# Kernel optimization log

Hardware: AMD Instinct MI355X
Metric: run time of the kernel (lower is better)

## Reference

```python
import jax, jax.numpy as jnp
import numpy as np

N_NODES = 100000
N_EDGES = 1600000
D = 128


def setup_inputs() -> dict:
    key = jax.random.key(0)
    ks = jax.random.split(key, 12)
    x = jax.random.normal(ks[0], (N_NODES, D), dtype=jnp.float32)
    edge_index = jax.random.randint(ks[1], (2, N_EDGES), 0, N_NODES, dtype=jnp.int64)
    s = 1.0 / np.sqrt(D)
    params = {}
    for i in range(3):
        params[f"Wl{i}"] = jax.random.uniform(ks[2 + 3 * i], (D, D), jnp.float32, -s, s)
        params[f"bl{i}"] = jax.random.uniform(ks[3 + 3 * i], (D,), jnp.float32, -s, s)
        params[f"Wr{i}"] = jax.random.uniform(ks[4 + 3 * i], (D, D), jnp.float32, -s, s)
    return {"x": x, "edge_index": edge_index, **params}


def _sage_conv(x, src, dst, Wl, bl, Wr):
    # mean-aggregate neighbor features: out_i = mean_{j: (j->i)} x_j
    msg = x[src]                                              # [E, D] gather
    agg = jax.ops.segment_sum(msg, dst, num_segments=N_NODES)  # [N, D]
    deg = jax.ops.segment_sum(jnp.ones_like(dst, dtype=x.dtype), dst, num_segments=N_NODES)
    agg = agg / jnp.maximum(deg, 1.0)[:, None]
    # PyG SAGEConv: lin_l(aggregated) + lin_r(x); lin_r has no bias
    return agg @ Wl + bl + x @ Wr


def reference(x, edge_index, Wl0, bl0, Wr0, Wl1, bl1, Wr1, Wl2, bl2, Wr2):
    src, dst = edge_index[0], edge_index[1]
    # layer 0 + relu (dropout is identity in eval mode)
    h = jax.nn.relu(_sage_conv(x, src, dst, Wl0, bl0, Wr0))
    # layer 1 + relu
    h = jax.nn.relu(_sage_conv(h, src, dst, Wl1, bl1, Wr1))
    # final layer, no activation
    return _sage_conv(h, src, dst, Wl2, bl2, Wr2)
```

## Files before the change

kernel.cpp:

```cpp
#include <hip/hip_runtime.h>
#include <hip/hip_bf16.h>

#define NN 100000
#define NE 1600000
#define DD 128

typedef __attribute__((ext_vector_type(8))) short bf16x8;
typedef __attribute__((ext_vector_type(4))) float f32x4;

__device__ __forceinline__ float bfu2f(unsigned short u) {
    unsigned v = ((unsigned)u) << 16;
    return __builtin_bit_cast(float, v);
}
__device__ __forceinline__ unsigned short f2bf(float f) {
    unsigned u = __builtin_bit_cast(unsigned, f);
    u += 0x7fffu + ((u >> 16) & 1u);
    return (unsigned short)(u >> 16);
}
__device__ __forceinline__ void split2(float v, unsigned short& hi, unsigned short& lo) {
    hi = f2bf(v);
    lo = f2bf(v - bfu2f(hi));
}
__device__ __forceinline__ float lo_f(unsigned u) { return __builtin_bit_cast(float, u << 16); }
__device__ __forceinline__ float hi_f(unsigned u) { return __builtin_bit_cast(float, u & 0xffff0000u); }

__global__ __launch_bounds__(256) void detect_kernel(const int* __restrict__ ei,
                                                     int* __restrict__ flag) {
    __shared__ int red[256];
    int t = threadIdx.x;
    int v = 0;
    for (int i = t; i < 4096; i += 256) v |= ei[2 * i + 1];
    red[t] = v;
    __syncthreads();
    for (int s = 128; s > 0; s >>= 1) {
        if (t < s) red[t] |= red[t + s];
        __syncthreads();
    }
    if (t == 0) flag[0] = (red[0] == 0) ? 1 : 0;
}

__device__ __forceinline__ int eidx(const int* __restrict__ ei, int idx, int is64) {
    return is64 ? ei[2 * idx] : ei[idx];
}

__global__ __launch_bounds__(256) void count_deg(const int* __restrict__ ei,
                                                 const int* __restrict__ flag,
                                                 int* __restrict__ deg) {
    int e = blockIdx.x * 256 + threadIdx.x;
    if (e < NE) {
        int is64 = flag[0];
        int dst = eidx(ei, NE + e, is64);
        atomicAdd(&deg[dst], 1);
    }
}

__global__ __launch_bounds__(1024) void scan_excl(const int* __restrict__ deg,
                                                  int* __restrict__ ptr) {
    __shared__ int wsum[16];
    __shared__ int carry_s;
    int t = threadIdx.x;
    int lane = t & 63, w = t >> 6;
    if (t == 0) carry_s = 0;
    __syncthreads();
    for (int base = 0; base < NN; base += 1024) {
        int i = base + t;
        int v = (i < NN) ? deg[i] : 0;
        int x = v;
        #pragma unroll
        for (int off = 1; off < 64; off <<= 1) {
            int y = __shfl_up(x, off, 64);
            if (lane >= off) x += y;
        }
        if (lane == 63) wsum[w] = x;
        __syncthreads();
        if (w == 0) {
            int s = (lane < 16) ? wsum[lane] : 0;
            #pragma unroll
            for (int off = 1; off < 16; off <<= 1) {
                int y = __shfl_up(s, off, 64);
                if (lane >= off) s += y;
            }
            if (lane < 16) wsum[lane] = s;
        }
        __syncthreads();
        int carry = carry_s;
        int woff = (w == 0) ? 0 : wsum[w - 1];
        if (i < NN) ptr[i] = carry + woff + (x - v);
        int chunk_total = wsum[15];
        __syncthreads();
        if (t == 0) carry_s = carry + chunk_total;
        __syncthreads();
    }
    if (threadIdx.x == 0) ptr[NN] = carry_s;
}

__global__ __launch_bounds__(256) void init_aux(const int* __restrict__ deg,
                                                const int* __restrict__ ptr,
                                                float* __restrict__ invd,
                                                int* __restrict__ cursor) {
    int i = blockIdx.x * 256 + threadIdx.x;
    if (i < NN) {
        int d = deg[i];
        invd[i] = 1.0f / (float)(d > 1 ? d : 1);
        cursor[i] = ptr[i];
    }
}

__global__ __launch_bounds__(256) void fill_csr(const int* __restrict__ ei,
                                                const int* __restrict__ flag,
                                                int* __restrict__ cursor,
                                                int* __restrict__ csre) {
    int e = blockIdx.x * 256 + threadIdx.x;
    if (e < NE) {
        int is64 = flag[0];
        int dst = eidx(ei, NE + e, is64);
        int src = eidx(ei, e, is64);
        int pos = atomicAdd(&cursor[dst], 1);
        csre[pos] = src;
    }
}

__global__ __launch_bounds__(256) void convert_x(const float* __restrict__ x,
                                                 unsigned* __restrict__ xh,
                                                 unsigned* __restrict__ xl) {
    int i = blockIdx.x * 256 + threadIdx.x;
    if (i >= NN * 64) return;
    float2 v = ((const float2*)x)[i];
    unsigned short h0, l0, h1, l1;
    split2(v.x, h0, l0);
    split2(v.y, h1, l1);
    xh[i] = (unsigned)h0 | ((unsigned)h1 << 16);
    xl[i] = (unsigned)l0 | ((unsigned)l1 << 16);
}

__global__ __launch_bounds__(256) void convert_w(const float* __restrict__ Wlm,
                                                 const float* __restrict__ Wrm,
                                                 unsigned short* __restrict__ Wth,
                                                 unsigned short* __restrict__ Wtl) {
    int i = blockIdx.x * 256 + threadIdx.x;
    if (i >= 128 * 256) return;
    int n = i >> 8, k = i & 255;
    float v = (k < 128) ? Wlm[k * 128 + n] : Wrm[(k - 128) * 128 + n];
    unsigned short h, l;
    split2(v, h, l);
    Wth[i] = h;
    Wtl[i] = l;
}

__global__ __launch_bounds__(256) void aggregate_bf(const unsigned* __restrict__ Hh,
                                                    const unsigned* __restrict__ Hl,
                                                    const int* __restrict__ csre,
                                                    const int* __restrict__ ptr,
                                                    const float* __restrict__ invd,
                                                    unsigned* __restrict__ Ah,
                                                    unsigned* __restrict__ Al) {
    int gw = blockIdx.x * 4 + (threadIdx.x >> 6);
    int lane = threadIdx.x & 63;
    if (gw >= NN) return;
    int beg = ptr[gw], end = ptr[gw + 1];
    float s00 = 0.f, s01 = 0.f, s10 = 0.f, s11 = 0.f;
    float s20 = 0.f, s21 = 0.f, s30 = 0.f, s31 = 0.f;
    int j = beg;
    for (; j + 4 <= end; j += 4) {
        int i0 = csre[j], i1 = csre[j + 1], i2 = csre[j + 2], i3 = csre[j + 3];
        unsigned h0 = Hh[(size_t)i0 * 64 + lane], g0 = Hl[(size_t)i0 * 64 + lane];
        unsigned h1 = Hh[(size_t)i1 * 64 + lane], g1 = Hl[(size_t)i1 * 64 + lane];
        unsigned h2 = Hh[(size_t)i2 * 64 + lane], g2 = Hl[(size_t)i2 * 64 + lane];
        unsigned h3 = Hh[(size_t)i3 * 64 + lane], g3 = Hl[(size_t)i3 * 64 + lane];
        s00 += lo_f(h0) + lo_f(g0); s01 += hi_f(h0) + hi_f(g0);
        s10 += lo_f(h1) + lo_f(g1); s11 += hi_f(h1) + hi_f(g1);
        s20 += lo_f(h2) + lo_f(g2); s21 += hi_f(h2) + hi_f(g2);
        s30 += lo_f(h3) + lo_f(g3); s31 += hi_f(h3) + hi_f(g3);
    }
    for (; j < end; ++j) {
        int i0 = csre[j];
        unsigned h0 = Hh[(size_t)i0 * 64 + lane], g0 = Hl[(size_t)i0 * 64 + lane];
        s00 += lo_f(h0) + lo_f(g0);
        s01 += hi_f(h0) + hi_f(g0);
    }
    float s = invd[gw];
    float v0 = ((s00 + s10) + (s20 + s30)) * s;
    float v1 = ((s01 + s11) + (s21 + s31)) * s;
    unsigned short h0_, l0_, h1_, l1_;
    split2(v0, h0_, l0_);
    split2(v1, h1_, l1_);
    Ah[(size_t)gw * 64 + lane] = (unsigned)h0_ | ((unsigned)h1_ << 16);
    Al[(size_t)gw * 64 + lane] = (unsigned)l0_ | ((unsigned)l1_ << 16);
}

__global__ __launch_bounds__(256) void gemm_mfma(const unsigned short* __restrict__ A0h,
                                                 const unsigned short* __restrict__ A0l,
                                                 const unsigned short* __restrict__ A1h,
                                                 const unsigned short* __restrict__ A1l,
                                                 const unsigned short* __restrict__ Wh,
                                                 const unsigned short* __restrict__ Wl_,
                                                 const float* __restrict__ bias,
                                                 unsigned short* __restrict__ Oh,
                                                 unsigned short* __restrict__ Ol,
                                                 float* __restrict__ Of,
                                                 int mode) {
    int t = threadIdx.x;
    int w = t >> 6, l = t & 63;
    int lr = l & 15, lh = l >> 4;
    int m0 = blockIdx.x * 64 + w * 16;
    int ra = m0 + lr;
    if (ra >= NN) ra = NN - 1;
    const char* pa0h = (const char*)A0h + (size_t)ra * 256;
    const char* pa0l = (const char*)A0l + (size_t)ra * 256;
    const char* pa1h = (const char*)A1h + (size_t)ra * 256;
    const char* pa1l = (const char*)A1l + (size_t)ra * 256;
    bf16x8 ah[8], al[8];
    #pragma unroll
    for (int s = 0; s < 4; ++s) {
        int off = s * 64 + lh * 16;
        ah[s]     = *(const bf16x8*)(pa0h + off);
        al[s]     = *(const bf16x8*)(pa0l + off);
        ah[s + 4] = *(const bf16x8*)(pa1h + off);
        al[s + 4] = *(const bf16x8*)(pa1l + off);
    }
    #pragma unroll
    for (int ct = 0; ct < 8; ++ct) {
        int colr = ct * 16 + lr;
        const char* pbh = (const char*)Wh + (size_t)colr * 512;
        const char* pbl = (const char*)Wl_ + (size_t)colr * 512;
        f32x4 acc = {0.f, 0.f, 0.f, 0.f};
        #pragma unroll
        for (int s = 0; s < 8; ++s) {
            int off = s * 64 + lh * 16;
            bf16x8 bh = *(const bf16x8*)(pbh + off);
            bf16x8 bl = *(const bf16x8*)(pbl + off);
            acc = __builtin_amdgcn_mfma_f32_16x16x32_bf16(ah[s], bh, acc, 0, 0, 0);
            acc = __builtin_amdgcn_mfma_f32_16x16x32_bf16(ah[s], bl, acc, 0, 0, 0);
            acc = __builtin_amdgcn_mfma_f32_16x16x32_bf16(al[s], bh, acc, 0, 0, 0);
        }
        float bv = bias[colr];
        #pragma unroll
        for (int r = 0; r < 4; ++r) {
            int row = m0 + lh * 4 + r;
            if (row < NN) {
                float v = acc[r] + bv;
                if (mode == 0) {
                    v = fmaxf(v, 0.f);
                    unsigned short hh, ll;
                    split2(v, hh, ll);
                    Oh[(size_t)row * 128 + colr] = hh;
                    Ol[(size_t)row * 128 + colr] = ll;
                } else {
                    Of[(size_t)row * 128 + colr] = v;
                }
            }
        }
    }
}

extern "C" void kernel_launch(void* const* d_in, const int* in_sizes, int n_in,
                              void* d_out, int out_size, void* d_ws, size_t ws_size,
                              hipStream_t stream) {
    const float* x   = (const float*)d_in[0];
    const int*   ei  = (const int*)d_in[1];
    const float* Wl0 = (const float*)d_in[2];
    const float* bl0 = (const float*)d_in[3];
    const float* Wr0 = (const float*)d_in[4];
    const float* Wl1 = (const float*)d_in[5];
    const float* bl1 = (const float*)d_in[6];
    const float* Wr1 = (const float*)d_in[7];
    const float* Wl2 = (const float*)d_in[8];
    const float* bl2 = (const float*)d_in[9];
    const float* Wr2 = (const float*)d_in[10];
    float* out = (float*)d_out;

    char* p = (char*)d_ws;
    auto alloc = [&](size_t bytes) {
        char* q = p;
        p += (bytes + 255) & ~(size_t)255;
        return q;
    };
    int*   deg    = (int*)alloc((size_t)NN * 4);
    int*   ptr    = (int*)alloc((size_t)(NN + 1) * 4);
    int*   cursor = (int*)alloc((size_t)NN * 4);
    int*   csre   = (int*)alloc((size_t)NE * 4);
    float* invd   = (float*)alloc((size_t)NN * 4);
    int*   flag   = (int*)alloc(256);
    unsigned short* Wth0 = (unsigned short*)alloc(128 * 256 * 2);
    unsigned short* Wtl0 = (unsigned short*)alloc(128 * 256 * 2);
    unsigned short* Wth1 = (unsigned short*)alloc(128 * 256 * 2);
    unsigned short* Wtl1 = (unsigned short*)alloc(128 * 256 * 2);
    unsigned short* Wth2 = (unsigned short*)alloc(128 * 256 * 2);
    unsigned short* Wtl2 = (unsigned short*)alloc(128 * 256 * 2);
    unsigned* xh   = (unsigned*)alloc((size_t)NN * 64 * 4);
    unsigned* xl   = (unsigned*)alloc((size_t)NN * 64 * 4);
    unsigned* aggh = (unsigned*)alloc((size_t)NN * 64 * 4);
    unsigned* aggl = (unsigned*)alloc((size_t)NN * 64 * 4);
    unsigned* h1h = (unsigned*)d_out;
    unsigned* h1l = h1h + (size_t)NN * 64;

    hipMemsetAsync(deg, 0, (size_t)NN * 4, stream);
    detect_kernel<<<1, 256, 0, stream>>>(ei, flag);
    count_deg<<<(NE + 255) / 256, 256, 0, stream>>>(ei, flag, deg);
    scan_excl<<<1, 1024, 0, stream>>>(deg, ptr);
    init_aux<<<(NN + 255) / 256, 256, 0, stream>>>(deg, ptr, invd, cursor);
    fill_csr<<<(NE + 255) / 256, 256, 0, stream>>>(ei, flag, cursor, csre);

    convert_x<<<(NN * 64 + 255) / 256, 256, 0, stream>>>(x, xh, xl);
    convert_w<<<128, 256, 0, stream>>>(Wl0, Wr0, Wth0, Wtl0);
    convert_w<<<128, 256, 0, stream>>>(Wl1, Wr1, Wth1, Wtl1);
    convert_w<<<128, 256, 0, stream>>>(Wl2, Wr2, Wth2, Wtl2);

    dim3 blk(256);
    dim3 gAgg(NN / 4);
    dim3 gGemm((NN + 63) / 64);

    aggregate_bf<<<gAgg, blk, 0, stream>>>(xh, xl, csre, ptr, invd, aggh, aggl);
    gemm_mfma<<<gGemm, blk, 0, stream>>>((unsigned short*)aggh, (unsigned short*)aggl,
                                         (unsigned short*)xh, (unsigned short*)xl,
                                         Wth0, Wtl0, bl0,
                                         (unsigned short*)h1h, (unsigned short*)h1l,
                                         nullptr, 0);
    aggregate_bf<<<gAgg, blk, 0, stream>>>(h1h, h1l, csre, ptr, invd, aggh, aggl);
    gemm_mfma<<<gGemm, blk, 0, stream>>>((unsigned short*)aggh, (unsigned short*)aggl,
                                         (unsigned short*)h1h, (unsigned short*)h1l,
                                         Wth1, Wtl1, bl1,
                                         (unsigned short*)xh, (unsigned short*)xl,
                                         nullptr, 0);
    aggregate_bf<<<gAgg, blk, 0, stream>>>(xh, xl, csre, ptr, invd, aggh, aggl);
    gemm_mfma<<<gGemm, blk, 0, stream>>>((unsigned short*)aggh, (unsigned short*)aggl,
                                         (unsigned short*)xh, (unsigned short*)xl,
                                         Wth2, Wtl2, bl2,
                                         nullptr, nullptr, out, 1);
}
```

Measured before the change: 1.117 ms.

## Interleave hi/lo bf16 halves per row and parallelize CSR offset scan

Stores the hi and lo bf16 split of each feature row contiguously in one 512-byte row instead of two separate arrays, so each gathered neighbor in aggregation is a single contiguous 8-byte-per-lane load covering both halves. The wave splits lanes between the hi and lo halves and combines them with a cross-half shuffle, with the neighbor loop unrolled by 8 for more loads in flight. The single-block sequential scan is replaced by a three-kernel multi-block scan that also fuses the init_aux work, and bias loads in the GEMM are hoisted. The risk is the extra shuffles and split work per lane in aggregation and the extra kernel launches for the scan.

```diff
diff --git a/kernel.cpp b/kernel.cpp
--- a/kernel.cpp
+++ b/kernel.cpp
@@ -7,6 +7,7 @@
 
 typedef __attribute__((ext_vector_type(8))) short bf16x8;
 typedef __attribute__((ext_vector_type(4))) float f32x4;
+
 
 __device__ __forceinline__ float bfu2f(unsigned short u) {
     unsigned v = ((unsigned)u) << 16;
@@ -54,56 +55,66 @@
     }
 }
 
-__global__ __launch_bounds__(1024) void scan_excl(const int* __restrict__ deg,
-                                                  int* __restrict__ ptr) {
-    __shared__ int wsum[16];
-    __shared__ int carry_s;
-    int t = threadIdx.x;
-    int lane = t & 63, w = t >> 6;
-    if (t == 0) carry_s = 0;
+__global__ __launch_bounds__(1024) void scan_part(const int* __restrict__ deg,
+                                                  int* __restrict__ ptr,
+                                                  int* __restrict__ bsum) {
+    __shared__ int ws[16];
+    int t = threadIdx.x, lane = t & 63, w = t >> 6;
+    int i = blockIdx.x * 1024 + t;
+    int v = (i < NN) ? deg[i] : 0;
+    int x = v;
+    #pragma unroll
+    for (int off = 1; off < 64; off <<= 1) {
+        int y = __shfl_up(x, off, 64);
+        if (lane >= off) x += y;
+    }
+    if (lane == 63) ws[w] = x;
     __syncthreads();
-    for (int base = 0; base < NN; base += 1024) {
-        int i = base + t;
-        int v = (i < NN) ? deg[i] : 0;
-        int x = v;
-        #pragma unroll
-        for (int off = 1; off < 64; off <<= 1) {
-            int y = __shfl_up(x, off, 64);
-            if (lane >= off) x += y;
+    if (w == 0) {
+        int s = (lane < 16) ? ws[lane] : 0;
+        #pragma unroll
+        for (int off = 1; off < 16; off <<= 1) {
+            int y = __shfl_up(s, off, 64);
+            if (lane >= off) s += y;
         }
-        if (lane == 63) wsum[w] = x;
-        __syncthreads();
-        if (w == 0) {
-            int s = (lane < 16) ? wsum[lane] : 0;
-            #pragma unroll
-            for (int off = 1; off < 16; off <<= 1) {
-                int y = __shfl_up(s, off, 64);
-                if (lane >= off) s += y;
-            }
-            if (lane < 16) wsum[lane] = s;
-        }
-        __syncthreads();
-        int carry = carry_s;
-        int woff = (w == 0) ? 0 : wsum[w - 1];
-        if (i < NN) ptr[i] = carry + woff + (x - v);
-        int chunk_total = wsum[15];
-        __syncthreads();
-        if (t == 0) carry_s = carry + chunk_total;
-        __syncthreads();
-    }
-    if (threadIdx.x == 0) ptr[NN] = carry_s;
-}
-
-__global__ __launch_bounds__(256) void init_aux(const int* __restrict__ deg,
-                                                const int* __restrict__ ptr,
-                                                float* __restrict__ invd,
-                                                int* __restrict__ cursor) {
+        if (lane < 16) ws[lane] = s;
+    }
+    __syncthreads();
+    int woff = (w == 0) ? 0 : ws[w - 1];
+    if (i < NN) ptr[i] = woff + (x - v);
+    if (t == 1023) bsum[blockIdx.x] = ws[15];
+}
+
+__global__ __launch_bounds__(128) void scan_top(int* __restrict__ bsum) {
+    __shared__ int wt[2];
+    int t = threadIdx.x, lane = t & 63, w = t >> 6;
+    int v = (t < 98) ? bsum[t] : 0;
+    int x = v;
+    #pragma unroll
+    for (int off = 1; off < 64; off <<= 1) {
+        int y = __shfl_up(x, off, 64);
+        if (lane >= off) x += y;
+    }
+    if (lane == 63) wt[w] = x;
+    __syncthreads();
+    int add = (w == 1) ? wt[0] : 0;
+    if (t < 98) bsum[t] = add + (x - v);
+}
+
+__global__ __launch_bounds__(256) void scan_final(const int* __restrict__ deg,
+                                                  const int* __restrict__ bsum,
+                                                  int* __restrict__ ptr,
+                                                  float* __restrict__ invd,
+                                                  int* __restrict__ cursor) {
     int i = blockIdx.x * 256 + threadIdx.x;
     if (i < NN) {
+        int p = ptr[i] + bsum[i >> 10];
+        ptr[i] = p;
+        cursor[i] = p;
         int d = deg[i];
         invd[i] = 1.0f / (float)(d > 1 ? d : 1);
-        cursor[i] = ptr[i];
-    }
+    }
+    if (blockIdx.x == 0 && threadIdx.x == 0) ptr[NN] = NE;
 }
 
 __global__ __launch_bounds__(256) void fill_csr(const int* __restrict__ ei,
@@ -121,16 +132,16 @@
 }
 
 __global__ __launch_bounds__(256) void convert_x(const float* __restrict__ x,
-                                                 unsigned* __restrict__ xh,
-                                                 unsigned* __restrict__ xl) {
+                                                 unsigned* __restrict__ H) {
     int i = blockIdx.x * 256 + threadIdx.x;
     if (i >= NN * 64) return;
     float2 v = ((const float2*)x)[i];
     unsigned short h0, l0, h1, l1;
     split2(v.x, h0, l0);
     split2(v.y, h1, l1);
-    xh[i] = (unsigned)h0 | ((unsigned)h1 << 16);
-    xl[i] = (unsigned)l0 | ((unsigned)l1 << 16);
+    int n = i >> 6, w = i & 63;
+    H[(size_t)n * 128 + w]      = (unsigned)h0 | ((unsigned)h1 << 16);
+    H[(size_t)n * 128 + 64 + w] = (unsigned)l0 | ((unsigned)l1 << 16);
 }
 
 __global__ __launch_bounds__(256) void convert_w(const float* __restrict__ Wlm,
@@ -147,56 +158,68 @@
     Wtl[i] = l;
 }
 
-__global__ __launch_bounds__(256) void aggregate_bf(const unsigned* __restrict__ Hh,
-                                                    const unsigned* __restrict__ Hl,
+__global__ __launch_bounds__(256) void aggregate_bf(const unsigned* __restrict__ H,
                                                     const int* __restrict__ csre,
                                                     const int* __restrict__ ptr,
                                                     const float* __restrict__ invd,
-                                                    unsigned* __restrict__ Ah,
-                                                    unsigned* __restrict__ Al) {
+                                                    unsigned* __restrict__ A) {
     int gw = blockIdx.x * 4 + (threadIdx.x >> 6);
     int lane = threadIdx.x & 63;
     if (gw >= NN) return;
     int beg = ptr[gw], end = ptr[gw + 1];
-    float s00 = 0.f, s01 = 0.f, s10 = 0.f, s11 = 0.f;
-    float s20 = 0.f, s21 = 0.f, s30 = 0.f, s31 = 0.f;
+    float s0 = 0.f, s1 = 0.f, s2 = 0.f, s3 = 0.f;
     int j = beg;
-    for (; j + 4 <= end; j += 4) {
-        int i0 = csre[j], i1 = csre[j + 1], i2 = csre[j + 2], i3 = csre[j + 3];
-        unsigned h0 = Hh[(size_t)i0 * 64 + lane], g0 = Hl[(size_t)i0 * 64 + lane];
-        unsigned h1 = Hh[(size_t)i1 * 64 + lane], g1 = Hl[(size_t)i1 * 64 + lane];
-        unsigned h2 = Hh[(size_t)i2 * 64 + lane], g2 = Hl[(size_t)i2 * 64 + lane];
-        unsigned h3 = Hh[(size_t)i3 * 64 + lane], g3 = Hl[(size_t)i3 * 64 + lane];
-        s00 += lo_f(h0) + lo_f(g0); s01 += hi_f(h0) + hi_f(g0);
-        s10 += lo_f(h1) + lo_f(g1); s11 += hi_f(h1) + hi_f(g1);
-        s20 += lo_f(h2) + lo_f(g2); s21 += hi_f(h2) + hi_f(g2);
-        s30 += lo_f(h3) + lo_f(g3); s31 += hi_f(h3) + hi_f(g3);
+    for (; j + 8 <= end; j += 8) {
+        int idx[8];
+        #pragma unroll
+        for (int q = 0; q < 8; ++q) idx[q] = csre[j + q];
+        uint2 r[8];
+        #pragma unroll
+        for (int q = 0; q < 8; ++q)
+            r[q] = *(const uint2*)(H + (size_t)idx[q] * 128 + lane * 2);
+        #pragma unroll
+        for (int q = 0; q < 8; ++q) {
+            s0 += lo_f(r[q].x);
+            s1 += hi_f(r[q].x);
+            s2 += lo_f(r[q].y);
+            s3 += hi_f(r[q].y);
+        }
     }
     for (; j < end; ++j) {
-        int i0 = csre[j];
-        unsigned h0 = Hh[(size_t)i0 * 64 + lane], g0 = Hl[(size_t)i0 * 64 + lane];
-        s00 += lo_f(h0) + lo_f(g0);
-        s01 += hi_f(h0) + hi_f(g0);
-    }
-    float s = invd[gw];
-    float v0 = ((s00 + s10) + (s20 + s30)) * s;
-    float v1 = ((s01 + s11) + (s21 + s31)) * s;
-    unsigned short h0_, l0_, h1_, l1_;
-    split2(v0, h0_, l0_);
-    split2(v1, h1_, l1_);
-    Ah[(size_t)gw * 64 + lane] = (unsigned)h0_ | ((unsigned)h1_ << 16);
-    Al[(size_t)gw * 64 + lane] = (unsigned)l0_ | ((unsigned)l1_ << 16);
-}
-
-__global__ __launch_bounds__(256) void gemm_mfma(const unsigned short* __restrict__ A0h,
-                                                 const unsigned short* __restrict__ A0l,
-                                                 const unsigned short* __restrict__ A1h,
-                                                 const unsigned short* __restrict__ A1l,
+        uint2 r = *(const uint2*)(H + (size_t)csre[j] * 128 + lane * 2);
+        s0 += lo_f(r.x);
+        s1 += hi_f(r.x);
+        s2 += lo_f(r.y);
+        s3 += hi_f(r.y);
+    }
+    s0 += __shfl_xor(s0, 32, 64);
+    s1 += __shfl_xor(s1, 32, 64);
+    s2 += __shfl_xor(s2, 32, 64);
+    s3 += __shfl_xor(s3, 32, 64);
+    float sc = invd[gw];
+    float t0 = s0 * sc, t1 = s1 * sc, t2 = s2 * sc, t3 = s3 * sc;
+    unsigned short h0, l0, h1, l1, h2, l2, h3, l3;
+    split2(t0, h0, l0);
+    split2(t1, h1, l1);
+    split2(t2, h2, l2);
+    split2(t3, h3, l3);
+    unsigned w0, w1;
+    if (lane < 32) {
+        w0 = (unsigned)h0 | ((unsigned)h1 << 16);
+        w1 = (unsigned)h2 | ((unsigned)h3 << 16);
+    } else {
+        w0 = (unsigned)l0 | ((unsigned)l1 << 16);
+        w1 = (unsigned)l2 | ((unsigned)l3 << 16);
+    }
+    *(uint2*)(A + (size_t)gw * 128 + lane * 2) = make_uint2(w0, w1);
+}
+
+__global__ __launch_bounds__(256) void gemm_mfma(const unsigned* __restrict__ A0,
+                                                 const unsigned* __restrict__ A1,
                                                  const unsigned short* __restrict__ Wh,
                                                  const unsigned short* __restrict__ Wl_,
                                                  const float* __restrict__ bias,
-                                                 unsigned short* __restrict__ Oh,
-                                                 unsigned short* __restrict__ Ol,
+                                                 unsigned* __restrict__ O,
                                                  float* __restrict__ Of,
                                                  int mode) {
     int t = threadIdx.x;
@@ -205,19 +228,20 @@
     int m0 = blockIdx.x * 64 + w * 16;
     int ra = m0 + lr;
     if (ra >= NN) ra = NN - 1;
-    const char* pa0h = (const char*)A0h + (size_t)ra * 256;
-    const char* pa0l = (const char*)A0l + (size_t)ra * 256;
-    const char* pa1h = (const char*)A1h + (size_t)ra * 256;
-    const char* pa1l = (const char*)A1l + (size_t)ra * 256;
+    const char* pa0 = (const char*)(A0 + (size_t)ra * 128);
+    const char* pa1 = (const char*)(A1 + (size_t)ra * 128);
     bf16x8 ah[8], al[8];
     #pragma unroll
     for (int s = 0; s < 4; ++s) {
         int off = s * 64 + lh * 16;
-        ah[s]     = *(const bf16x8*)(pa0h + off);
-        al[s]     = *(const bf16x8*)(pa0l + off);
-        ah[s + 4] = *(const bf16x8*)(pa1h + off);
-        al[s + 4] = *(const bf16x8*)(pa1l + off);
-    }
+        ah[s]     = *(const bf16x8*)(pa0 + off);
+        al[s]     = *(const bf16x8*)(pa0 + 256 + off);
+        ah[s + 4] = *(const bf16x8*)(pa1 + off);
+        al[s + 4] = *(const bf16x8*)(pa1 + 256 + off);
+    }
+    float bv[8];
+    #pragma unroll
+    for (int ct = 0; ct < 8; ++ct) bv[ct] = bias[ct * 16 + lr];
     #pragma unroll
     for (int ct = 0; ct < 8; ++ct) {
         int colr = ct * 16 + lr;
@@ -233,18 +257,18 @@
             acc = __builtin_amdgcn_mfma_f32_16x16x32_bf16(ah[s], bl, acc, 0, 0, 0);
             acc = __builtin_amdgcn_mfma_f32_16x16x32_bf16(al[s], bh, acc, 0, 0, 0);
         }
-        float bv = bias[colr];
         #pragma unroll
         for (int r = 0; r < 4; ++r) {
             int row = m0 + lh * 4 + r;
             if (row < NN) {
-                float v = acc[r] + bv;
+                float v = acc[r] + bv[ct];
                 if (mode == 0) {
                     v = fmaxf(v, 0.f);
                     unsigned short hh, ll;
                     split2(v, hh, ll);
-                    Oh[(size_t)row * 128 + colr] = hh;
-                    Ol[(size_t)row * 128 + colr] = ll;
+                    char* po = (char*)(O + (size_t)row * 128);
+                    *(unsigned short*)(po + colr * 2) = hh;
+                    *(unsigned short*)(po + 256 + colr * 2) = ll;
                 } else {
                     Of[(size_t)row * 128 + colr] = v;
                 }
@@ -281,27 +305,26 @@
     int*   csre   = (int*)alloc((size_t)NE * 4);
     float* invd   = (float*)alloc((size_t)NN * 4);
     int*   flag   = (int*)alloc(256);
+    int*   bsum   = (int*)alloc(128 * 4);
     unsigned short* Wth0 = (unsigned short*)alloc(128 * 256 * 2);
     unsigned short* Wtl0 = (unsigned short*)alloc(128 * 256 * 2);
     unsigned short* Wth1 = (unsigned short*)alloc(128 * 256 * 2);
     unsigned short* Wtl1 = (unsigned short*)alloc(128 * 256 * 2);
     unsigned short* Wth2 = (unsigned short*)alloc(128 * 256 * 2);
     unsigned short* Wtl2 = (unsigned short*)alloc(128 * 256 * 2);
-    unsigned* xh   = (unsigned*)alloc((size_t)NN * 64 * 4);
-    unsigned* xl   = (unsigned*)alloc((size_t)NN * 64 * 4);
-    unsigned* aggh = (unsigned*)alloc((size_t)NN * 64 * 4);
-    unsigned* aggl = (unsigned*)alloc((size_t)NN * 64 * 4);
-    unsigned* h1h = (unsigned*)d_out;
-    unsigned* h1l = h1h + (size_t)NN * 64;
+    unsigned* xH   = (unsigned*)alloc((size_t)NN * 128 * 4);
+    unsigned* aggH = (unsigned*)alloc((size_t)NN * 128 * 4);
+    unsigned* h1H = (unsigned*)d_out;
 
     hipMemsetAsync(deg, 0, (size_t)NN * 4, stream);
     detect_kernel<<<1, 256, 0, stream>>>(ei, flag);
     count_deg<<<(NE + 255) / 256, 256, 0, stream>>>(ei, flag, deg);
-    scan_excl<<<1, 1024, 0, stream>>>(deg, ptr);
-    init_aux<<<(NN + 255) / 256, 256, 0, stream>>>(deg, ptr, invd, cursor);
+    scan_part<<<(NN + 1023) / 1024, 1024, 0, stream>>>(deg, ptr, bsum);
+    scan_top<<<1, 128, 0, stream>>>(bsum);
+    scan_final<<<(NN + 255) / 256, 256, 0, stream>>>(deg, bsum, ptr, invd, cursor);
     fill_csr<<<(NE + 255) / 256, 256, 0, stream>>>(ei, flag, cursor, csre);
 
-    convert_x<<<(NN * 64 + 255) / 256, 256, 0, stream>>>(x, xh, xl);
+    convert_x<<<(NN * 64 + 255) / 256, 256, 0, stream>>>(x, xH);
     convert_w<<<128, 256, 0, stream>>>(Wl0, Wr0, Wth0, Wtl0);
     convert_w<<<128, 256, 0, stream>>>(Wl1, Wr1, Wth1, Wtl1);
     convert_w<<<128, 256, 0, stream>>>(Wl2, Wr2, Wth2, Wtl2);
@@ -310,21 +333,10 @@
     dim3 gAgg(NN / 4);
     dim3 gGemm((NN + 63) / 64);
 
-    aggregate_bf<<<gAgg, blk, 0, stream>>>(xh, xl, csre, ptr, invd, aggh, aggl);
-    gemm_mfma<<<gGemm, blk, 0, stream>>>((unsigned short*)aggh, (unsigned short*)aggl,
-                                         (unsigned short*)xh, (unsigned short*)xl,
-                                         Wth0, Wtl0, bl0,
-                                         (unsigned short*)h1h, (unsigned short*)h1l,
-                                         nullptr, 0);
-    aggregate_bf<<<gAgg, blk, 0, stream>>>(h1h, h1l, csre, ptr, invd, aggh, aggl);
-    gemm_mfma<<<gGemm, blk, 0, stream>>>((unsigned short*)aggh, (unsigned short*)aggl,
-                                         (unsigned short*)h1h, (unsigned short*)h1l,
-                                         Wth1, Wtl1, bl1,
-                                         (unsigned short*)xh, (unsigned short*)xl,
-                                         nullptr, 0);
-    aggregate_bf<<<gAgg, blk, 0, stream>>>(xh, xl, csre, ptr, invd, aggh, aggl);
-    gemm_mfma<<<gGemm, blk, 0, stream>>>((unsigned short*)aggh, (unsigned short*)aggl,
-                                         (unsigned short*)xh, (unsigned short*)xl,
-                                         Wth2, Wtl2, bl2,
-                                         nullptr, nullptr, out, 1);
-}
+    aggregate_bf<<<gAgg, blk, 0, stream>>>(xH, csre, ptr, invd, aggH);
+    gemm_mfma<<<gGemm, blk, 0, stream>>>(aggH, xH, Wth0, Wtl0, bl0, h1H, nullptr, 0);
+    aggregate_bf<<<gAgg, blk, 0, stream>>>(h1H, csre, ptr, invd, aggH);
+    gemm_mfma<<<gGemm, blk, 0, stream>>>(aggH, h1H, Wth1, Wtl1, bl1, xH, nullptr, 0);
+    aggregate_bf<<<gAgg, blk, 0, stream>>>(xH, csre, ptr, invd, aggH);
+    gemm_mfma<<<gGemm, blk, 0, stream>>>(aggH, xH, Wth2, Wtl2, bl2, nullptr, out, 1);
+}
```

After: 1.006 ms. 9.9% less time.
